# Kernel optimization log

Hardware: AMD Instinct MI355X
Metric: run time of the kernel (lower is better)

Reference implementation:

```python
import jax, jax.numpy as jnp
import numpy as np

EMBED_DIM = 1024
NUM_HEADS = 16
HEAD_DIM = EMBED_DIM // NUM_HEADS
ROPE_BASE = 10000.0


def rotate_half(x):
    d = x.shape[-1] // 2
    x1, x2 = x[..., :d], x[..., d:]
    return jnp.concatenate((-x2, x1), axis=-1)


def setup_inputs() -> dict:
    key = jax.random.key(0)
    k_x, k_wqkv, k_bqkv, k_wo, k_bo = jax.random.split(key, 5)
    C = EMBED_DIM
    x = jax.random.normal(k_x, (4, 2048, C), dtype=jnp.float32)
    s = 1.0 / np.sqrt(C)
    W_qkv = jax.random.uniform(k_wqkv, (C, 3 * C), minval=-s, maxval=s, dtype=jnp.float32)
    b_qkv = jax.random.uniform(k_bqkv, (3 * C,), minval=-s, maxval=s, dtype=jnp.float32)
    W_out = jax.random.uniform(k_wo, (C, C), minval=-s, maxval=s, dtype=jnp.float32)
    b_out = jax.random.uniform(k_bo, (C,), minval=-s, maxval=s, dtype=jnp.float32)
    return {"x": x, "W_qkv": W_qkv, "b_qkv": b_qkv, "W_out": W_out, "b_out": b_out}


def reference(x, W_qkv, b_qkv, W_out, b_out):
    B, T, C = x.shape
    H, Dh = NUM_HEADS, HEAD_DIM
    # fused QKV projection: [B,T,3C] -> [3,B,H,T,Dh]
    qkv = (x @ W_qkv + b_qkv).reshape(B, T, 3, H, Dh).transpose(2, 0, 3, 1, 4)
    q, k, v = qkv[0], qkv[1], qkv[2]
    # rotary embedding: freqs [T, Dh/2] -> emb [T, Dh]
    inv_freq = 1.0 / (ROPE_BASE ** (jnp.arange(0, Dh, 2, dtype=jnp.float32) / Dh))
    freqs = jnp.arange(T, dtype=jnp.float32)[:, None] * inv_freq[None, :]
    emb = jnp.concatenate((freqs, freqs), axis=-1)  # [T, Dh], broadcasts over B,H
    cos, sin = jnp.cos(emb), jnp.sin(emb)
    q = q * cos + rotate_half(q) * sin
    k = k * cos + rotate_half(k) * sin
    # full (non-causal) attention, manual softmax
    scale = 1.0 / np.sqrt(Dh)
    attn = jax.nn.softmax(jnp.einsum("bhqd,bhkd->bhqk", q, k) * scale, axis=-1)
    out = jnp.einsum("bhqk,bhkd->bhqd", attn, v)  # [B,H,T,Dh]
    out = out.transpose(0, 2, 1, 3).reshape(B, T, C)
    return out @ W_out + b_out
```

## Files before the change

kernel.cpp:

```cpp
#include <hip/hip_runtime.h>
#include <math.h>

#define T_SEQ 2048
#define CDIM  1024
#define NH    16
#define DHD   64
#define BATCH 4
#define MROWS (BATCH * T_SEQ)
#define BHN   (BATCH * NH)

typedef _Float16 f16;
typedef __attribute__((ext_vector_type(8))) _Float16 f16x8;
typedef __attribute__((ext_vector_type(4))) _Float16 f16x4;
typedef __attribute__((ext_vector_type(2))) _Float16 f16x2;
typedef __attribute__((ext_vector_type(2))) __fp16 fp16x2;
typedef __attribute__((ext_vector_type(4))) float f32x4;

__device__ __forceinline__ float fast_exp2(float x) {
#if __has_builtin(__builtin_amdgcn_exp2f)
    return __builtin_amdgcn_exp2f(x);
#else
    return exp2f(x);
#endif
}

__device__ __forceinline__ f16x2 cvt_pk_f16(float a, float b) {
    fp16x2 r = __builtin_amdgcn_cvt_pkrtz(a, b);
    return __builtin_bit_cast(f16x2, r);
}

__device__ __forceinline__ void gl_lds16(const f16* g, f16* l) {
    __builtin_amdgcn_global_load_lds(
        (const __attribute__((address_space(1))) void*)(g),
        (__attribute__((address_space(3))) void*)(l),
        16, 0, 0);
}

__global__ void rope_tables_kernel(float* __restrict__ ctab, float* __restrict__ stab)
{
    int idx = blockIdx.x * 256 + threadIdx.x;
    int t = idx >> 5, i = idx & 31;
    double inv = pow(10000.0, -(double)(2 * i) / 64.0);
    double a = (double)t * inv;
    ctab[idx] = (float)cos(a);
    stab[idx] = (float)sin(a);
}

__global__ __launch_bounds__(256) void xcvt_kernel(
    const float* __restrict__ X, f16* __restrict__ Xf)
{
    int idx = blockIdx.x * 256 + threadIdx.x;
    const float4* src = (const float4*)X + (size_t)idx * 2;
    float4 a = src[0], b = src[1];
    f16x8 o;
    o[0] = (f16)a.x; o[1] = (f16)a.y; o[2] = (f16)a.z; o[3] = (f16)a.w;
    o[4] = (f16)b.x; o[5] = (f16)b.y; o[6] = (f16)b.z; o[7] = (f16)b.w;
    *((f16x8*)Xf + idx) = o;
}

__global__ __launch_bounds__(64) void wcvt_kernel(
    const float* __restrict__ W, f16* __restrict__ Wt, int N)
{
    int lane = threadIdx.x;
    int k0 = blockIdx.x * 8;
    int n = blockIdx.y * 64 + lane;
    f16x8 o;
#pragma unroll
    for (int j = 0; j < 8; j++) o[j] = (f16)W[(size_t)(k0 + j) * N + n];
    *(f16x8*)(Wt + (size_t)n * CDIM + k0) = o;
}

#define GEMM_MAINLOOP(Aimg, Bimg, M0, N0)                                         \
    __shared__ f16 As[128][32], Bs[128][32];                                      \
    const int tid = threadIdx.x, wave = tid >> 6, lane = tid & 63;                \
    const int l16 = lane & 15, quad = lane >> 4;                                  \
    const int wm = wave >> 1, wn = wave & 1;                                      \
    f32x4 acc[4][4];                                                              \
    _Pragma("unroll") for (int i = 0; i < 4; i++)                                 \
        _Pragma("unroll") for (int j = 0; j < 4; j++)                             \
            acc[i][j] = (f32x4){0.f, 0.f, 0.f, 0.f};                              \
    const f16* sbase = (wave < 2) ? (Aimg) : (Bimg);                              \
    f16* lbase = ((wave < 2) ? &As[0][0] : &Bs[0][0]) + (wave & 1) * 2048;        \
    const size_t srow0 = ((wave < 2) ? (size_t)(M0) : (size_t)(N0)) + (wave & 1) * 64; \
    const int srow = lane >> 2, schunk = (lane & 3) << 3;                         \
    for (int k0 = 0; k0 < CDIM; k0 += 32) {                                       \
        _Pragma("unroll") for (int it = 0; it < 4; it++)                          \
            gl_lds16(sbase + (srow0 + it * 16 + srow) * CDIM + k0 + schunk,       \
                     lbase + it * 512);                                           \
        __syncthreads();                                                          \
        f16x8 fa[4], fb[4];                                                       \
        _Pragma("unroll") for (int mi = 0; mi < 4; mi++)                          \
            fa[mi] = *(const f16x8*)&As[wm * 64 + mi * 16 + l16][quad * 8];       \
        _Pragma("unroll") for (int ni = 0; ni < 4; ni++)                          \
            fb[ni] = *(const f16x8*)&Bs[wn * 64 + ni * 16 + l16][quad * 8];       \
        _Pragma("unroll") for (int mi = 0; mi < 4; mi++)                          \
            _Pragma("unroll") for (int ni = 0; ni < 4; ni++)                      \
                acc[mi][ni] = __builtin_amdgcn_mfma_f32_16x16x32_f16(             \
                    fa[mi], fb[ni], acc[mi][ni], 0, 0, 0);                        \
        __syncthreads();                                                          \
    }

__global__ __launch_bounds__(256) void qkv_gemm_kernel(
    const f16* __restrict__ Xf, const f16* __restrict__ Wt,
    const float* __restrict__ bias,
    const float* __restrict__ ctab, const float* __restrict__ stab,
    f16* __restrict__ qf, f16* __restrict__ kf, f16* __restrict__ vf)
{
    const int m0 = blockIdx.x * 128;
    const int n0 = blockIdx.y * 128;
    GEMM_MAINLOOP(Xf, Wt, m0, n0)

    const int ncol0 = n0 + wn * 64;
    const int w = ncol0 >> 10;
    const int h = (ncol0 >> 6) & 15;
    const int b = m0 >> 11;
    const int trow0 = (m0 & 2047) + wm * 64 + quad * 4;
    float bia[4];
#pragma unroll
    for (int ni = 0; ni < 4; ni++) bia[ni] = bias[ncol0 + ni * 16 + l16];

    if (w < 2) {
        f16* oq = w ? kf : qf;
        const float sc = w ? 1.0f : 0.18033688011112042f;
#pragma unroll
        for (int mi = 0; mi < 4; mi++) {
#pragma unroll
            for (int i = 0; i < 4; i++) {
                int t = trow0 + mi * 16 + i;
                size_t rowoff = ((size_t)(b * NH + h) * T_SEQ + t) * DHD;
#pragma unroll
                for (int np = 0; np < 2; np++) {
                    int d = np * 16 + l16;
                    float v0 = acc[mi][np][i] + bia[np];
                    float v1 = acc[mi][np + 2][i] + bia[np + 2];
                    float c = ctab[(t << 5) + d];
                    float s = stab[(t << 5) + d];
                    oq[rowoff + d]      = (f16)((v0 * c - v1 * s) * sc);
                    oq[rowoff + d + 32] = (f16)((v1 * c + v0 * s) * sc);
                }
            }
        }
    } else {
#pragma unroll
        for (int mi = 0; mi < 4; mi++) {
#pragma unroll
            for (int i = 0; i < 4; i++) {
                int t = trow0 + mi * 16 + i;
                size_t rowoff = ((size_t)(b * NH + h) * T_SEQ + t) * DHD;
#pragma unroll
                for (int ni = 0; ni < 4; ni++)
                    vf[rowoff + ni * 16 + l16] = (f16)(acc[mi][ni][i] + bia[ni]);
            }
        }
    }
}

__global__ __launch_bounds__(256) void vt_kernel(
    const f16* __restrict__ vf, f16* __restrict__ vt)
{
    __shared__ f16 Ls[64][72];
    const int tid = threadIdx.x;
    const int tb = blockIdx.x;
    const int bh = blockIdx.y;
#pragma unroll
    for (int p = 0; p < 2; p++) {
        int idx = tid + p * 256;
        int r = idx >> 3, c8 = (idx & 7) << 3;
        *(f16x8*)&Ls[r][c8] =
            *(const f16x8*)(vf + ((size_t)bh * T_SEQ + tb * 64 + r) * DHD + c8);
    }
    __syncthreads();
#pragma unroll
    for (int p = 0; p < 2; p++) {
        int idx = tid + p * 256;
        int d = idx >> 3, t8 = (idx & 7) << 3;
        f16x8 o;
#pragma unroll
        for (int j = 0; j < 8; j++) o[j] = Ls[t8 + j][d];
        *(f16x8*)(vt + ((size_t)bh * DHD + d) * T_SEQ + (size_t)tb * 64 + t8) = o;
    }
}

__global__ __launch_bounds__(256, 4) void attn_kernel(
    const f16* __restrict__ qf, const f16* __restrict__ kf,
    const f16* __restrict__ vt, f16* __restrict__ ab)
{
    __shared__ f16 Kb[2][64][64];
    __shared__ f16 Vb[2][64][64];
    __shared__ f16 Pb[4][32][32];

    const int tid  = threadIdx.x;
    const int wave = tid >> 6, lane = tid & 63;
    const int l16  = lane & 15, quad = lane >> 4;

    const int flat = blockIdx.x + (blockIdx.y << 4);
    const int swz  = (flat & 7) * 128 + (flat >> 3);
    const int qt = swz & 15;
    const int bh = swz >> 4;
    const int q0 = qt * 128 + wave * 32;

    const f16* kbase = kf + (size_t)bh * T_SEQ * DHD;
    const f16* vbase = vt + (size_t)bh * DHD * T_SEQ;

    f16x8 qfr[2][2];
#pragma unroll
    for (int qs = 0; qs < 2; qs++) {
        const f16* qrow = qf + ((size_t)bh * T_SEQ + q0 + qs * 16 + l16) * DHD;
        qfr[qs][0] = *(const f16x8*)(qrow + quad * 8);
        qfr[qs][1] = *(const f16x8*)(qrow + 32 + quad * 8);
    }

    f32x4 o[2][4];
    f32x4 lacc[2];
#pragma unroll
    for (int qs = 0; qs < 2; qs++) {
        lacc[qs] = (f32x4){0.f, 0.f, 0.f, 0.f};
#pragma unroll
        for (int dt = 0; dt < 4; dt++) o[qs][dt] = (f32x4){0.f, 0.f, 0.f, 0.f};
    }
    f16x8 ones;
#pragma unroll
    for (int j = 0; j < 8; j++) ones[j] = (f16)1.0f;

    const int srow = tid >> 3;
    const int scw  = tid & 7;
    const int scol = scw << 3;
    const int swzc = (scw ^ (srow & 7)) << 3;

    const int prot = l16 & 14;

    f16x8 kreg[2], vreg[2];
#pragma unroll
    for (int r = 0; r < 2; r++) {
        kreg[r] = *(const f16x8*)(kbase + (size_t)(srow + r * 32) * DHD + scol);
        vreg[r] = *(const f16x8*)(vbase + (size_t)(srow + r * 32) * T_SEQ + scol);
    }
#pragma unroll
    for (int r = 0; r < 2; r++) {
        *(f16x8*)&Kb[0][srow + r * 32][swzc] = kreg[r];
        *(f16x8*)&Vb[0][srow + r * 32][swzc] = vreg[r];
    }
    __syncthreads();

    for (int kt = 0; kt < 32; kt++) {
        const int buf = kt & 1;
        if (kt < 31) {
#pragma unroll
            for (int r = 0; r < 2; r++) {
                kreg[r] = *(const f16x8*)(kbase + (size_t)((kt + 1) * 64 + srow + r * 32) * DHD + scol);
                vreg[r] = *(const f16x8*)(vbase + (size_t)(srow + r * 32) * T_SEQ + (kt + 1) * 64 + scol);
            }
        }

#pragma unroll
        for (int half = 0; half < 2; half++) {
            f32x4 sc[2][2];
#pragma unroll
            for (int k2 = 0; k2 < 2; k2++)
#pragma unroll
                for (int qs = 0; qs < 2; qs++) sc[k2][qs] = (f32x4){0.f, 0.f, 0.f, 0.f};
#pragma unroll
            for (int k2 = 0; k2 < 2; k2++) {
                const int keyt = half * 2 + k2;
#pragma unroll
                for (int ks = 0; ks < 2; ks++) {
                    const int kc = ((ks * 4 + quad) ^ (l16 & 7)) << 3;
                    f16x8 kfr = *(const f16x8*)&Kb[buf][keyt * 16 + l16][kc];
#pragma unroll
                    for (int qs = 0; qs < 2; qs++)
                        sc[k2][qs] = __builtin_amdgcn_mfma_f32_16x16x32_f16(
                            kfr, qfr[qs][ks], sc[k2][qs], 0, 0, 0);
                }
            }
#pragma unroll
            for (int k2 = 0; k2 < 2; k2++) {
#pragma unroll
                for (int qs = 0; qs < 2; qs++) {
                    f16x2 pa = cvt_pk_f16(
                        fast_exp2(sc[k2][qs][0]), fast_exp2(sc[k2][qs][1]));
                    f16x2 pb = cvt_pk_f16(
                        fast_exp2(sc[k2][qs][2]), fast_exp2(sc[k2][qs][3]));
                    f16x4 pv;
                    ((f16x2*)&pv)[0] = pa;
                    ((f16x2*)&pv)[1] = pb;
                    const int pc = (((k2 << 3) + (quad << 1) + prot) & 15) << 1;
                    *(f16x4*)&Pb[wave][qs * 16 + l16][pc] = pv;
                }
            }
            const int pr0 = (((quad << 2)     + prot) & 15) << 1;
            const int pr1 = (((quad << 2) + 2 + prot) & 15) << 1;
            f16x8 pfr[2];
#pragma unroll
            for (int qs = 0; qs < 2; qs++) {
                f16x4 plo = *(const f16x4*)&Pb[wave][qs * 16 + l16][pr0];
                f16x4 phi = *(const f16x4*)&Pb[wave][qs * 16 + l16][pr1];
                f16x8 pf;
                pf[0] = plo[0]; pf[1] = plo[1]; pf[2] = plo[2]; pf[3] = plo[3];
                pf[4] = phi[0]; pf[5] = phi[1]; pf[6] = phi[2]; pf[7] = phi[3];
                pfr[qs] = pf;
                lacc[qs] = __builtin_amdgcn_mfma_f32_16x16x32_f16(
                    pfr[qs], ones, lacc[qs], 0, 0, 0);
            }
#pragma unroll
            for (int dt = 0; dt < 4; dt++) {
                const int vc = ((half * 4 + quad) ^ (l16 & 7)) << 3;
                f16x8 vfr = *(const f16x8*)&Vb[buf][dt * 16 + l16][vc];
#pragma unroll
                for (int qs = 0; qs < 2; qs++)
                    o[qs][dt] = __builtin_amdgcn_mfma_f32_16x16x32_f16(
                        pfr[qs], vfr, o[qs][dt], 0, 0, 0);
            }
        }

        if (kt < 31) {
#pragma unroll
            for (int r = 0; r < 2; r++) {
                *(f16x8*)&Kb[buf ^ 1][srow + r * 32][swzc] = kreg[r];
                *(f16x8*)&Vb[buf ^ 1][srow + r * 32][swzc] = vreg[r];
            }
        }
        __syncthreads();
    }

    const int b = bh >> 4, h = bh & 15;
#pragma unroll
    for (int qs = 0; qs < 2; qs++) {
#pragma unroll
        for (int i = 0; i < 4; i++) {
            float iv = 1.f / lacc[qs][i];
            int m = b * T_SEQ + qt * 128 + wave * 32 + qs * 16 + quad * 4 + i;
#pragma unroll
            for (int dt = 0; dt < 4; dt++)
                ab[(size_t)m * CDIM + h * 64 + dt * 16 + l16] = (f16)(o[qs][dt][i] * iv);
        }
    }
}

__global__ __launch_bounds__(256) void out_gemm_kernel(
    const f16* __restrict__ Ab, const f16* __restrict__ Wt,
    const float* __restrict__ bias, float* __restrict__ out)
{
    const int m0 = blockIdx.x * 128;
    const int n0 = blockIdx.y * 128;
    GEMM_MAINLOOP(Ab, Wt, m0, n0)

    const int ncol0 = n0 + wn * 64;
    float bia[4];
#pragma unroll
    for (int ni = 0; ni < 4; ni++) bia[ni] = bias[ncol0 + ni * 16 + l16];
#pragma unroll
    for (int mi = 0; mi < 4; mi++) {
#pragma unroll
        for (int i = 0; i < 4; i++) {
            int m = m0 + wm * 64 + mi * 16 + quad * 4 + i;
#pragma unroll
            for (int ni = 0; ni < 4; ni++)
                out[(size_t)m * CDIM + ncol0 + ni * 16 + l16] = acc[mi][ni][i] + bia[ni];
        }
    }
}

extern "C" void kernel_launch(void* const* d_in, const int* in_sizes, int n_in,
                              void* d_out, int out_size, void* d_ws, size_t ws_size,
                              hipStream_t stream)
{
    const float* x    = (const float*)d_in[0];
    const float* Wqkv = (const float*)d_in[1];
    const float* bqkv = (const float*)d_in[2];
    const float* Wout = (const float*)d_in[3];
    const float* bout = (const float*)d_in[4];
    float* out = (float*)d_out;

    const size_t XSZ  = (size_t)MROWS * CDIM;
    const size_t WQSZ = (size_t)3072 * CDIM;
    const size_t WOSZ = (size_t)CDIM * CDIM;
    const size_t QSZ  = (size_t)BHN * T_SEQ * DHD;

    char* p = (char*)d_ws;
    f16* Xf  = (f16*)p; p += XSZ * 2;
    f16* Wqt = (f16*)p; p += WQSZ * 2;
    f16* Wot = (f16*)p; p += WOSZ * 2;
    f16* qf  = (f16*)p; p += QSZ * 2;
    f16* kf  = (f16*)p; p += QSZ * 2;
    f16* vf  = (f16*)p; p += QSZ * 2;
    f16* vtb = (f16*)p; p += QSZ * 2;
    f16* ab  = (f16*)p; p += QSZ * 2;
    float* ctab = (float*)p; p += T_SEQ * 32 * 4;
    float* stab = (float*)p; p += T_SEQ * 32 * 4;

    rope_tables_kernel<<<256, 256, 0, stream>>>(ctab, stab);
    xcvt_kernel<<<(int)(XSZ / 8 / 256), 256, 0, stream>>>(x, Xf);
    wcvt_kernel<<<dim3(128, 48), 64, 0, stream>>>(Wqkv, Wqt, 3072);
    wcvt_kernel<<<dim3(128, 16), 64, 0, stream>>>(Wout, Wot, 1024);
    qkv_gemm_kernel<<<dim3(64, 24), 256, 0, stream>>>(
        Xf, Wqt, bqkv, ctab, stab, qf, kf, vf);
    vt_kernel<<<dim3(32, BHN), 256, 0, stream>>>(vf, vtb);
    attn_kernel<<<dim3(16, BHN), 256, 0, stream>>>(qf, kf, vtb, ab);
    out_gemm_kernel<<<dim3(64, 8), 256, 0, stream>>>(ab, Wot, bout, out);
}
```

Baseline: 297.4 us.

## Fuse V transpose into QKV epilogue, merge weight converts, add MFMA priority hints

```diff
diff --git a/kernel.cpp b/kernel.cpp
--- a/kernel.cpp
+++ b/kernel.cpp
@@ -24,6 +24,14 @@
 #endif
 }
 
+__device__ __forceinline__ float fast_rcp(float x) {
+#if __has_builtin(__builtin_amdgcn_rcpf)
+    return __builtin_amdgcn_rcpf(x);
+#else
+    return 1.0f / x;
+#endif
+}
+
 __device__ __forceinline__ f16x2 cvt_pk_f16(float a, float b) {
     fp16x2 r = __builtin_amdgcn_cvt_pkrtz(a, b);
     return __builtin_bit_cast(f16x2, r);
@@ -59,11 +67,17 @@
 }
 
 __global__ __launch_bounds__(64) void wcvt_kernel(
-    const float* __restrict__ W, f16* __restrict__ Wt, int N)
+    const float* __restrict__ Wq, const float* __restrict__ Wo,
+    f16* __restrict__ Wqt, f16* __restrict__ Wot)
 {
     int lane = threadIdx.x;
     int k0 = blockIdx.x * 8;
-    int n = blockIdx.y * 64 + lane;
+    int ny = blockIdx.y;
+    const float* W;
+    f16* Wt;
+    int N, n;
+    if (ny < 48) { W = Wq; Wt = Wqt; N = 3072; n = ny * 64 + lane; }
+    else         { W = Wo; Wt = Wot; N = 1024; n = (ny - 48) * 64 + lane; }
     f16x8 o;
 #pragma unroll
     for (int j = 0; j < 8; j++) o[j] = (f16)W[(size_t)(k0 + j) * N + n];
@@ -104,7 +118,7 @@
     const f16* __restrict__ Xf, const f16* __restrict__ Wt,
     const float* __restrict__ bias,
     const float* __restrict__ ctab, const float* __restrict__ stab,
-    f16* __restrict__ qf, f16* __restrict__ kf, f16* __restrict__ vf)
+    f16* __restrict__ qf, f16* __restrict__ kf, f16* __restrict__ vtb)
 {
     const int m0 = blockIdx.x * 128;
     const int n0 = blockIdx.y * 128;
@@ -143,41 +157,16 @@
     } else {
 #pragma unroll
         for (int mi = 0; mi < 4; mi++) {
-#pragma unroll
-            for (int i = 0; i < 4; i++) {
-                int t = trow0 + mi * 16 + i;
-                size_t rowoff = ((size_t)(b * NH + h) * T_SEQ + t) * DHD;
-#pragma unroll
-                for (int ni = 0; ni < 4; ni++)
-                    vf[rowoff + ni * 16 + l16] = (f16)(acc[mi][ni][i] + bia[ni]);
-            }
-        }
-    }
-}
-
-__global__ __launch_bounds__(256) void vt_kernel(
-    const f16* __restrict__ vf, f16* __restrict__ vt)
-{
-    __shared__ f16 Ls[64][72];
-    const int tid = threadIdx.x;
-    const int tb = blockIdx.x;
-    const int bh = blockIdx.y;
-#pragma unroll
-    for (int p = 0; p < 2; p++) {
-        int idx = tid + p * 256;
-        int r = idx >> 3, c8 = (idx & 7) << 3;
-        *(f16x8*)&Ls[r][c8] =
-            *(const f16x8*)(vf + ((size_t)bh * T_SEQ + tb * 64 + r) * DHD + c8);
-    }
-    __syncthreads();
-#pragma unroll
-    for (int p = 0; p < 2; p++) {
-        int idx = tid + p * 256;
-        int d = idx >> 3, t8 = (idx & 7) << 3;
-        f16x8 o;
-#pragma unroll
-        for (int j = 0; j < 8; j++) o[j] = Ls[t8 + j][d];
-        *(f16x8*)(vt + ((size_t)bh * DHD + d) * T_SEQ + (size_t)tb * 64 + t8) = o;
+            const int tb = trow0 + mi * 16;
+#pragma unroll
+            for (int ni = 0; ni < 4; ni++) {
+                const int d = ni * 16 + l16;
+                f16x4 pv;
+#pragma unroll
+                for (int i = 0; i < 4; i++) pv[i] = (f16)(acc[mi][ni][i] + bia[ni]);
+                *(f16x4*)(vtb + ((size_t)(b * NH + h) * DHD + d) * T_SEQ + tb) = pv;
+            }
+        }
     }
 }
 
@@ -229,17 +218,22 @@
 
     const int prot = l16 & 14;
 
+    const f16* kp = kbase + (size_t)srow * DHD + scol;
+    const f16* vp = vbase + (size_t)srow * T_SEQ + scol;
+
     f16x8 kreg[2], vreg[2];
 #pragma unroll
     for (int r = 0; r < 2; r++) {
-        kreg[r] = *(const f16x8*)(kbase + (size_t)(srow + r * 32) * DHD + scol);
-        vreg[r] = *(const f16x8*)(vbase + (size_t)(srow + r * 32) * T_SEQ + scol);
+        kreg[r] = *(const f16x8*)(kp + (size_t)(r * 32) * DHD);
+        vreg[r] = *(const f16x8*)(vp + (size_t)(r * 32) * T_SEQ);
     }
 #pragma unroll
     for (int r = 0; r < 2; r++) {
         *(f16x8*)&Kb[0][srow + r * 32][swzc] = kreg[r];
         *(f16x8*)&Vb[0][srow + r * 32][swzc] = vreg[r];
     }
+    const f16* kq = kp + 64 * DHD;
+    const f16* vq = vp + 64;
     __syncthreads();
 
     for (int kt = 0; kt < 32; kt++) {
@@ -247,9 +241,11 @@
         if (kt < 31) {
 #pragma unroll
             for (int r = 0; r < 2; r++) {
-                kreg[r] = *(const f16x8*)(kbase + (size_t)((kt + 1) * 64 + srow + r * 32) * DHD + scol);
-                vreg[r] = *(const f16x8*)(vbase + (size_t)(srow + r * 32) * T_SEQ + (kt + 1) * 64 + scol);
-            }
+                kreg[r] = *(const f16x8*)(kq + (size_t)(r * 32) * DHD);
+                vreg[r] = *(const f16x8*)(vq + (size_t)(r * 32) * T_SEQ);
+            }
+            kq += 64 * DHD;
+            vq += 64;
         }
 
 #pragma unroll
@@ -259,6 +255,7 @@
             for (int k2 = 0; k2 < 2; k2++)
 #pragma unroll
                 for (int qs = 0; qs < 2; qs++) sc[k2][qs] = (f32x4){0.f, 0.f, 0.f, 0.f};
+            __builtin_amdgcn_s_setprio(1);
 #pragma unroll
             for (int k2 = 0; k2 < 2; k2++) {
                 const int keyt = half * 2 + k2;
@@ -272,6 +269,7 @@
                             kfr, qfr[qs][ks], sc[k2][qs], 0, 0, 0);
                 }
             }
+            __builtin_amdgcn_s_setprio(0);
 #pragma unroll
             for (int k2 = 0; k2 < 2; k2++) {
 #pragma unroll
@@ -298,9 +296,12 @@
                 pf[0] = plo[0]; pf[1] = plo[1]; pf[2] = plo[2]; pf[3] = plo[3];
                 pf[4] = phi[0]; pf[5] = phi[1]; pf[6] = phi[2]; pf[7] = phi[3];
                 pfr[qs] = pf;
+            }
+            __builtin_amdgcn_s_setprio(1);
+#pragma unroll
+            for (int qs = 0; qs < 2; qs++)
                 lacc[qs] = __builtin_amdgcn_mfma_f32_16x16x32_f16(
                     pfr[qs], ones, lacc[qs], 0, 0, 0);
-            }
 #pragma unroll
             for (int dt = 0; dt < 4; dt++) {
                 const int vc = ((half * 4 + quad) ^ (l16 & 7)) << 3;
@@ -310,6 +311,7 @@
                     o[qs][dt] = __builtin_amdgcn_mfma_f32_16x16x32_f16(
                         pfr[qs], vfr, o[qs][dt], 0, 0, 0);
             }
+            __builtin_amdgcn_s_setprio(0);
         }
 
         if (kt < 31) {
@@ -327,7 +329,7 @@
     for (int qs = 0; qs < 2; qs++) {
 #pragma unroll
         for (int i = 0; i < 4; i++) {
-            float iv = 1.f / lacc[qs][i];
+            float iv = fast_rcp(lacc[qs][i]);
             int m = b * T_SEQ + qt * 128 + wave * 32 + qs * 16 + quad * 4 + i;
 #pragma unroll
             for (int dt = 0; dt < 4; dt++)
@@ -382,7 +384,6 @@
     f16* Wot = (f16*)p; p += WOSZ * 2;
     f16* qf  = (f16*)p; p += QSZ * 2;
     f16* kf  = (f16*)p; p += QSZ * 2;
-    f16* vf  = (f16*)p; p += QSZ * 2;
     f16* vtb = (f16*)p; p += QSZ * 2;
     f16* ab  = (f16*)p; p += QSZ * 2;
     float* ctab = (float*)p; p += T_SEQ * 32 * 4;
@@ -390,11 +391,9 @@
 
     rope_tables_kernel<<<256, 256, 0, stream>>>(ctab, stab);
     xcvt_kernel<<<(int)(XSZ / 8 / 256), 256, 0, stream>>>(x, Xf);
-    wcvt_kernel<<<dim3(128, 48), 64, 0, stream>>>(Wqkv, Wqt, 3072);
-    wcvt_kernel<<<dim3(128, 16), 64, 0, stream>>>(Wout, Wot, 1024);
+    wcvt_kernel<<<dim3(128, 64), 64, 0, stream>>>(Wqkv, Wout, Wqt, Wot);
     qkv_gemm_kernel<<<dim3(64, 24), 256, 0, stream>>>(
-        Xf, Wqt, bqkv, ctab, stab, qf, kf, vf);
-    vt_kernel<<<dim3(32, BHN), 256, 0, stream>>>(vf, vtb);
+        Xf, Wqt, bqkv, ctab, stab, qf, kf, vtb);
     attn_kernel<<<dim3(16, BHN), 256, 0, stream>>>(qf, kf, vtb, ab);
     out_gemm_kernel<<<dim3(64, 8), 256, 0, stream>>>(ab, Wot, bout, out);
 }
```

Measured after the change: 294.7 us. No clear change (-0.9%).
